# Kernel tuning notes

Measured on AMD Instinct MI355X. Metric: run time of the kernel, lower is better.

Reference implementation:

```python
import jax, jax.numpy as jnp
import numpy as np

EMBED = 1024
HEADS = 16
HEAD_DIM = EMBED // HEADS
N, L = 2, 2048


def setup_inputs() -> dict:
    key = jax.random.key(0)
    ks = jax.random.split(key, 9)
    s = 0.02
    return {
        "values": jax.random.normal(ks[0], (N, L, EMBED), jnp.float32),
        "key": jax.random.normal(ks[1], (N, L, EMBED), jnp.float32),
        "query": jax.random.normal(ks[2], (N, L, EMBED), jnp.float32),
        "mask": jnp.ones((N, 1, 1, L), jnp.int32),
        "Wv": jax.random.normal(ks[3], (HEAD_DIM, HEAD_DIM), jnp.float32) * s,
        "Wk": jax.random.normal(ks[4], (HEAD_DIM, HEAD_DIM), jnp.float32) * s,
        "Wq": jax.random.normal(ks[5], (HEAD_DIM, HEAD_DIM), jnp.float32) * s,
        "bq": jax.random.normal(ks[6], (HEAD_DIM,), jnp.float32) * s,
        "Wo": jax.random.normal(ks[7], (EMBED, EMBED), jnp.float32) * s,
        "bo": jax.random.normal(ks[8], (EMBED,), jnp.float32) * s,
    }


def reference(values, key, query, mask, Wv, Wk, Wq, bq, Wo, bo):
    n, q_len, E = query.shape
    D = Wv.shape[0]
    H = E // D
    # split heads: (N, len, H, D)
    v = values.reshape(n, -1, H, D)
    k = key.reshape(n, -1, H, D)
    q = query.reshape(n, q_len, H, D)
    # per-head linear projections (torch Linear: x @ W.T [+ b])
    v = jnp.einsum("nlhd,ed->nlhe", v, Wv)
    k = jnp.einsum("nlhd,ed->nlhe", k, Wk)
    q = jnp.einsum("nlhd,ed->nlhe", q, Wq) + bq
    # scores: (N, H, q_len, k_len)
    energy = jnp.einsum("nqhd,nkhd->nhqk", q, k)
    energy = jnp.where(mask == 0, jnp.float32(-1e20), energy)
    # NOTE: original scales by sqrt(embed_size), not sqrt(head_dim)
    attn = jax.nn.softmax(energy / jnp.sqrt(jnp.float32(E)), axis=-1)
    out = jnp.einsum("nhqk,nkhd->nqhd", attn, v).reshape(n, q_len, E)
    return out @ Wo.T + bo
```

## Files before the change

### kernel.cpp

```cpp
#include <hip/hip_runtime.h>
#include <hip/hip_bf16.h>
#include <string.h>

#define NB   2
#define SEQ  2048
#define EMB  1024
#define NH   16
#define HD   64
#define QSCALE 0.045084219f
#define MADD2  -4.5084219e18f

typedef __attribute__((ext_vector_type(8))) short short8;
typedef __attribute__((ext_vector_type(4))) float f32x4;

#define MFMA(a, b, c) __builtin_amdgcn_mfma_f32_16x16x32_bf16(a, b, c, 0, 0, 0)
#define EXP2(x) __builtin_amdgcn_exp2f(x)

__device__ __forceinline__ unsigned short f2bf(float x) {
    union { float f; unsigned u; } v; v.f = x;
    unsigned r = v.u + 0x7fffu + ((v.u >> 16) & 1u);
    return (unsigned short)(r >> 16);
}
__device__ __forceinline__ unsigned packbf2(float a, float b) {
    __hip_bfloat162 h = __float22bfloat162_rn(make_float2(a, b));
    unsigned u; memcpy(&u, &h, 4);
    return u;
}
__device__ __forceinline__ void gload16(const void* g, void* l) {
    __builtin_amdgcn_global_load_lds(
        (const __attribute__((address_space(1))) void*)g,
        (__attribute__((address_space(3))) void*)l, 16, 0, 0);
}

__global__ __launch_bounds__(256) void cvt_kernel(
    const float* __restrict__ Wo, const float* __restrict__ Wq,
    const float* __restrict__ Wk, const float* __restrict__ Wv,
    const int* __restrict__ mask,
    unsigned short* __restrict__ Wob, unsigned short* __restrict__ Wqb,
    unsigned short* __restrict__ Wkb, unsigned short* __restrict__ Wvb,
    float* __restrict__ maddG)
{
    const int b = blockIdx.x, tid = threadIdx.x;
    if (b < 1024) {
        int idx = b * 256 + tid;
        float4 w = ((const float4*)Wo)[idx];
        uint2 p; p.x = packbf2(w.x, w.y); p.y = packbf2(w.z, w.w);
        ((uint2*)Wob)[idx] = p;
    } else if (b < 1027) {
        const float* W = (b == 1024) ? Wq : (b == 1025) ? Wk : Wv;
        unsigned short* Wb = (b == 1024) ? Wqb : (b == 1025) ? Wkb : Wvb;
        #pragma unroll
        for (int i = 0; i < 4; ++i) {
            int idx = tid + i * 256;
            float4 w = ((const float4*)W)[idx];
            uint2 p; p.x = packbf2(w.x, w.y); p.y = packbf2(w.z, w.w);
            ((uint2*)Wb)[idx] = p;
        }
    } else {
        #pragma unroll
        for (int i = 0; i < 16; ++i) {
            int idx = tid + i * 256;
            maddG[idx] = mask[idx] ? 0.f : MADD2;
        }
    }
}

__global__ __launch_bounds__(256) void qkv_kernel(
    const float* __restrict__ Qin, const float* __restrict__ Kin,
    const float* __restrict__ Vin,
    const unsigned short* __restrict__ Wqb, const unsigned short* __restrict__ Wkb,
    const unsigned short* __restrict__ Wvb, const float* __restrict__ bq,
    unsigned short* __restrict__ Qp, unsigned short* __restrict__ Kp,
    unsigned short* __restrict__ Vtp)
{
    const int lt = blockIdx.x;
    const int h  = blockIdx.y;
    const int tz = blockIdx.z;
    const int t  = tz >> 1, n = tz & 1;

    const float* X; const unsigned short* Wb;
    if (t == 0)      { X = Qin; Wb = Wqb; }
    else if (t == 1) { X = Kin; Wb = Wkb; }
    else             { X = Vin; Wb = Wvb; }

    __shared__ __align__(16) unsigned short sX[128][70];
    __shared__ __align__(16) unsigned short sT[64][136];

    const int tid = threadIdx.x, wave = tid >> 6, lane = tid & 63;
    const int ln = lane & 15, quad = lane >> 4;

    #pragma unroll
    for (int i = 0; i < 8; ++i) {
        int flat = tid + i * 256;
        int r = flat >> 4, c4 = flat & 15;
        float4 xv = *(const float4*)(X + ((size_t)(n * SEQ + lt * 128 + r)) * EMB + h * HD + c4 * 4);
        uint2 xp; xp.x = packbf2(xv.x, xv.y); xp.y = packbf2(xv.z, xv.w);
        *(uint2*)&sX[r][c4 * 4] = xp;
    }
    short8 wf0[4], wf1[4];
    #pragma unroll
    for (int nt = 0; nt < 4; ++nt) {
        wf0[nt] = *(const short8*)(Wb + (nt * 16 + ln) * HD + quad * 8);
        wf1[nt] = *(const short8*)(Wb + (nt * 16 + ln) * HD + 32 + quad * 8);
    }
    __syncthreads();

    f32x4 acc[2][4];
    #pragma unroll
    for (int set = 0; set < 2; ++set) {
        short8 af0 = *(const short8*)&sX[wave * 32 + set * 16 + ln][quad * 8];
        short8 af1 = *(const short8*)&sX[wave * 32 + set * 16 + ln][32 + quad * 8];
        #pragma unroll
        for (int nt = 0; nt < 4; ++nt) {
            f32x4 a = {0.f, 0.f, 0.f, 0.f};
            a = MFMA(af0, wf0[nt], a);
            a = MFMA(af1, wf1[nt], a);
            acc[set][nt] = a;
        }
    }

    if (t == 0) {
        #pragma unroll
        for (int nt = 0; nt < 4; ++nt) {
            float bb = bq[nt * 16 + ln];
            #pragma unroll
            for (int set = 0; set < 2; ++set)
                #pragma unroll
                for (int a = 0; a < 4; ++a)
                    acc[set][nt][a] = (acc[set][nt][a] + bb) * QSCALE;
        }
    }

    if (t < 2) {
        unsigned short* Out = (t == 0) ? Qp : Kp;
        #pragma unroll
        for (int set = 0; set < 2; ++set)
            #pragma unroll
            for (int a = 0; a < 4; ++a) {
                size_t row = (size_t)((n * NH + h) * SEQ + lt * 128 + wave * 32 + set * 16 + quad * 4 + a);
                #pragma unroll
                for (int nt = 0; nt < 4; ++nt)
                    Out[row * HD + nt * 16 + ln] = f2bf(acc[set][nt][a]);
            }
    } else {
        #pragma unroll
        for (int set = 0; set < 2; ++set)
            #pragma unroll
            for (int nt = 0; nt < 4; ++nt)
                #pragma unroll
                for (int a = 0; a < 4; ++a)
                    sT[nt * 16 + ln][wave * 32 + set * 16 + quad * 4 + a] = f2bf(acc[set][nt][a]);
        __syncthreads();
        #pragma unroll
        for (int i = 0; i < 4; ++i) {
            int flat = tid + i * 256;
            int r = flat >> 4, c8 = flat & 15;
            *(float4*)(Vtp + ((size_t)((n * NH + h) * HD + r)) * SEQ + lt * 128 + c8 * 8) =
                *(const float4*)&sT[r][c8 * 8];
        }
    }
}

__global__ __launch_bounds__(256) void flash_kernel(
    const unsigned short* __restrict__ Qp, const unsigned short* __restrict__ Kp,
    const unsigned short* __restrict__ Vtp, const float* __restrict__ maddG,
    unsigned short* __restrict__ A )
{
    const int nh = blockIdx.x;
    const int qt = blockIdx.y;
    const int n  = nh >> 4, h = nh & 15;

    const int tid  = threadIdx.x;
    const int wave = tid >> 6, lane = tid & 63;
    const int ln   = lane & 15, quad = lane >> 4;
    const int ln7  = lane & 7;

    __shared__ __align__(16) unsigned short Kb[2][64 * 64];
    __shared__ __align__(16) unsigned short Vb[2][64 * 64];
    __shared__ __align__(16) unsigned short sP[4][32 * 64];
    unsigned short* sPw = sP[wave];

    const unsigned short* Qb = Qp + ((size_t)nh * SEQ + qt * 128 + wave * 32) * HD;
    short8 qf[2][2];
    #pragma unroll
    for (int set = 0; set < 2; ++set) {
        qf[set][0] = *(const short8*)(Qb + (set * 16 + ln) * HD + quad * 8);
        qf[set][1] = *(const short8*)(Qb + (set * 16 + ln) * HD + 32 + quad * 8);
    }

    const unsigned short* Kg = Kp  + (size_t)nh * SEQ * HD;
    const unsigned short* Vg = Vtp + (size_t)nh * HD * SEQ;
    const float* mb = maddG + n * SEQ;

    const int r8  = lane >> 3;
    const int swz = ((lane & 7) ^ r8) << 3;

    f32x4 o[2][4];
    #pragma unroll
    for (int s2 = 0; s2 < 2; ++s2)
        #pragma unroll
        for (int dt = 0; dt < 4; ++dt) o[s2][dt] = (f32x4){0.f, 0.f, 0.f, 0.f};
    float lsum[2] = {0.f, 0.f};

    #define STAGE(buf, kt_) do {                                                  \
        const unsigned short* kg_ = Kg + ((size_t)((kt_) * 64 + wave * 16 + r8)) * HD + swz; \
        const unsigned short* vg_ = Vg + ((size_t)(wave * 16 + r8)) * SEQ + (kt_) * 64 + swz; \
        unsigned short* kl_ = &Kb[buf][wave * 16 * 64];                           \
        unsigned short* vl_ = &Vb[buf][wave * 16 * 64];                           \
        gload16(kg_,            kl_);                                             \
        gload16(kg_ + 8 * HD,   kl_ + 8 * 64);                                    \
        gload16(vg_,            vl_);                                             \
        gload16(vg_ + 8 * SEQ,  vl_ + 8 * 64);                                    \
    } while (0)

    STAGE(0, 0);
    __syncthreads();
    int cur = 0;

    for (int kt = 0; kt < SEQ / 64; ++kt) {
        float4 md[4];
        #pragma unroll
        for (int nt = 0; nt < 4; ++nt)
            md[nt] = *(const float4*)(mb + kt * 64 + nt * 16 + quad * 4);

        if (kt + 1 < SEQ / 64) STAGE(cur ^ 1, kt + 1);

        const unsigned short* Kc = Kb[cur];
        #pragma unroll
        for (int nt = 0; nt < 4; ++nt) {
            short8 kf0 = *(const short8*)&Kc[(nt * 16 + ln) * 64 + (((quad)     ^ ln7) << 3)];
            short8 kf1 = *(const short8*)&Kc[(nt * 16 + ln) * 64 + (((quad + 4) ^ ln7) << 3)];
            #pragma unroll
            for (int set = 0; set < 2; ++set) {
                f32x4 z = {0.f, 0.f, 0.f, 0.f};
                z = MFMA(kf0, qf[set][0], z);
                z = MFMA(kf1, qf[set][1], z);
                float p0 = EXP2(fminf(z[0] + md[nt].x, 80.f));
                float p1 = EXP2(fminf(z[1] + md[nt].y, 80.f));
                float p2 = EXP2(fminf(z[2] + md[nt].z, 80.f));
                float p3 = EXP2(fminf(z[3] + md[nt].w, 80.f));
                lsum[set] += (p0 + p1) + (p2 + p3);
                uint2 w; w.x = packbf2(p0, p1); w.y = packbf2(p2, p3);
                int prow  = set * 16 + ln;
                int chunk = nt * 2 + (quad >> 1);
                *(uint2*)&sPw[prow * 64 + ((chunk ^ ln7) << 3) + (quad & 1) * 4] = w;
            }
        }
        asm volatile("s_waitcnt lgkmcnt(0)" ::: "memory");

        const unsigned short* Vc = Vb[cur];
        short8 pf[2][2];
        #pragma unroll
        for (int set = 0; set < 2; ++set) {
            pf[set][0] = *(const short8*)&sPw[(set * 16 + ln) * 64 + (((quad)     ^ ln7) << 3)];
            pf[set][1] = *(const short8*)&sPw[(set * 16 + ln) * 64 + (((quad + 4) ^ ln7) << 3)];
        }
        #pragma unroll
        for (int dt = 0; dt < 4; ++dt) {
            short8 vf0 = *(const short8*)&Vc[(dt * 16 + ln) * 64 + (((quad)     ^ ln7) << 3)];
            short8 vf1 = *(const short8*)&Vc[(dt * 16 + ln) * 64 + (((quad + 4) ^ ln7) << 3)];
            #pragma unroll
            for (int set = 0; set < 2; ++set) {
                o[set][dt] = MFMA(pf[set][0], vf0, o[set][dt]);
                o[set][dt] = MFMA(pf[set][1], vf1, o[set][dt]);
            }
        }

        __syncthreads();
        cur ^= 1;
    }
    #undef STAGE

    #pragma unroll
    for (int set = 0; set < 2; ++set) {
        float l = lsum[set];
        l += __shfl_xor(l, 16);
        l += __shfl_xor(l, 32);
        #pragma unroll
        for (int a = 0; a < 4; ++a) {
            float inv = 1.0f / __shfl(l, quad * 4 + a);
            size_t row = (size_t)(n * SEQ + qt * 128 + wave * 32 + set * 16 + quad * 4 + a);
            #pragma unroll
            for (int dt = 0; dt < 4; ++dt)
                A[row * EMB + h * HD + dt * 16 + ln] = f2bf(o[set][dt][a] * inv);
        }
    }
}

__global__ __launch_bounds__(256) void outproj_kernel(
    const unsigned short* __restrict__ A, const unsigned short* __restrict__ Wob,
    const float* __restrict__ bo, float* __restrict__ Out)
{
    const int ct = blockIdx.x;
    const int rt = blockIdx.y;

    const int tid  = threadIdx.x;
    const int wave = tid >> 6, lane = tid & 63;
    const int ln   = lane & 15, quad = lane >> 4;
    const int wm   = wave >> 1, wn = wave & 1;

    __shared__ __align__(16) unsigned short sA[128][72];
    __shared__ __align__(16) unsigned short sB[128][72];

    f32x4 acc[4][4];
    #pragma unroll
    for (int i = 0; i < 4; ++i)
        #pragma unroll
        for (int j = 0; j < 4; ++j) acc[i][j] = (f32x4){0.f, 0.f, 0.f, 0.f};

    for (int kc = 0; kc < EMB / 64; ++kc) {
        __syncthreads();
        #pragma unroll
        for (int i = 0; i < 4; ++i) {
            int flat = tid + i * 256;
            int r = flat >> 3, c8 = flat & 7;
            *(float4*)&sA[r][c8 * 8] =
                *(const float4*)(A + (size_t)(rt * 128 + r) * EMB + kc * 64 + c8 * 8);
            *(float4*)&sB[r][c8 * 8] =
                *(const float4*)(Wob + (size_t)(ct * 128 + r) * EMB + kc * 64 + c8 * 8);
        }
        __syncthreads();

        #pragma unroll
        for (int ks = 0; ks < 2; ++ks) {
            short8 af[4], bf[4];
            #pragma unroll
            for (int i = 0; i < 4; ++i)
                af[i] = *(const short8*)&sA[wm * 64 + i * 16 + ln][ks * 32 + quad * 8];
            #pragma unroll
            for (int j = 0; j < 4; ++j)
                bf[j] = *(const short8*)&sB[wn * 64 + j * 16 + ln][ks * 32 + quad * 8];
            #pragma unroll
            for (int i = 0; i < 4; ++i)
                #pragma unroll
                for (int j = 0; j < 4; ++j)
                    acc[i][j] = MFMA(af[i], bf[j], acc[i][j]);
        }
    }

    #pragma unroll
    for (int j = 0; j < 4; ++j) {
        int col = ct * 128 + wn * 64 + j * 16 + ln;
        float bb = bo[col];
        #pragma unroll
        for (int i = 0; i < 4; ++i)
            #pragma unroll
            for (int a = 0; a < 4; ++a) {
                size_t row = (size_t)(rt * 128 + wm * 64 + i * 16 + quad * 4 + a);
                Out[row * EMB + col] = acc[i][j][a] + bb;
            }
    }
}

extern "C" void kernel_launch(void* const* d_in, const int* in_sizes, int n_in,
                              void* d_out, int out_size, void* d_ws, size_t ws_size,
                              hipStream_t stream) {
    const float* values = (const float*)d_in[0];
    const float* key_   = (const float*)d_in[1];
    const float* query  = (const float*)d_in[2];
    const int*   mask   = (const int*)d_in[3];
    const float* Wv     = (const float*)d_in[4];
    const float* Wk     = (const float*)d_in[5];
    const float* Wq     = (const float*)d_in[6];
    const float* bq     = (const float*)d_in[7];
    const float* Wo     = (const float*)d_in[8];
    const float* bo     = (const float*)d_in[9];
    float* out = (float*)d_out;

    const size_t NHLD = (size_t)NB * NH * SEQ * HD;

    unsigned short* ws = (unsigned short*)d_ws;
    unsigned short* Qp    = ws;
    unsigned short* Kp    = ws + NHLD;
    unsigned short* Vtp   = ws + 2 * NHLD;
    unsigned short* Aattn = ws + 3 * NHLD;
    unsigned short* Wob   = ws + 4 * NHLD;
    unsigned short* Wqb   = Wob + (size_t)EMB * EMB;
    unsigned short* Wkb   = Wqb + HD * HD;
    unsigned short* Wvb   = Wkb + HD * HD;
    float* maddG = (float*)(Wvb + HD * HD);

    cvt_kernel<<<dim3(1028), 256, 0, stream>>>(
        Wo, Wq, Wk, Wv, mask, Wob, Wqb, Wkb, Wvb, maddG);
    qkv_kernel<<<dim3(SEQ / 128, NH, 3 * NB), 256, 0, stream>>>(
        query, key_, values, Wqb, Wkb, Wvb, bq, Qp, Kp, Vtp);
    flash_kernel<<<dim3(NB * NH, SEQ / 128), 256, 0, stream>>>(
        Qp, Kp, Vtp, maddG, Aattn);
    outproj_kernel<<<dim3(EMB / 128, NB * SEQ / 128), 256, 0, stream>>>(
        Aattn, Wob, bo, out);
}
```

Baseline: 205.1 us.

## Apply key mask by zeroing V rows and computing row sums with MFMA

Instead of adding a large negative bias before exp2 and clamping, the flash kernel now exponentiates raw scores. It applies the mask by zeroing masked rows of V in the projection kernel. It also computes the softmax denominator as P times a bf16 0/1 mask vector on the matrix cores. This removes the per-element add, min and scalar sum plus the final cross-lane shuffles from the inner loop, at the cost of extra MFMAs. Dropping the clamp risks overflow if scores are large, and the denominator is now summed from bf16-rounded probabilities.

```diff
diff --git a/kernel.cpp b/kernel.cpp
--- a/kernel.cpp
+++ b/kernel.cpp
@@ -8,7 +8,6 @@
 #define NH   16
 #define HD   64
 #define QSCALE 0.045084219f
-#define MADD2  -4.5084219e18f
 
 typedef __attribute__((ext_vector_type(8))) short short8;
 typedef __attribute__((ext_vector_type(4))) float f32x4;
@@ -38,7 +37,7 @@
     const int* __restrict__ mask,
     unsigned short* __restrict__ Wob, unsigned short* __restrict__ Wqb,
     unsigned short* __restrict__ Wkb, unsigned short* __restrict__ Wvb,
-    float* __restrict__ maddG)
+    unsigned short* __restrict__ Mb)
 {
     const int b = blockIdx.x, tid = threadIdx.x;
     if (b < 1024) {
@@ -60,7 +59,7 @@
         #pragma unroll
         for (int i = 0; i < 16; ++i) {
             int idx = tid + i * 256;
-            maddG[idx] = mask[idx] ? 0.f : MADD2;
+            Mb[idx] = mask[idx] ? (unsigned short)0x3F80 : (unsigned short)0;
         }
     }
 }
@@ -70,6 +69,7 @@
     const float* __restrict__ Vin,
     const unsigned short* __restrict__ Wqb, const unsigned short* __restrict__ Wkb,
     const unsigned short* __restrict__ Wvb, const float* __restrict__ bq,
+    const int* __restrict__ mask,
     unsigned short* __restrict__ Qp, unsigned short* __restrict__ Kp,
     unsigned short* __restrict__ Vtp)
 {
@@ -146,6 +146,16 @@
         #pragma unroll
         for (int set = 0; set < 2; ++set)
             #pragma unroll
+            for (int a = 0; a < 4; ++a) {
+                int l = lt * 128 + wave * 32 + set * 16 + quad * 4 + a;
+                if (mask[n * SEQ + l] == 0) {
+                    #pragma unroll
+                    for (int nt = 0; nt < 4; ++nt) acc[set][nt][a] = 0.f;
+                }
+            }
+        #pragma unroll
+        for (int set = 0; set < 2; ++set)
+            #pragma unroll
             for (int nt = 0; nt < 4; ++nt)
                 #pragma unroll
                 for (int a = 0; a < 4; ++a)
@@ -163,7 +173,7 @@
 
 __global__ __launch_bounds__(256) void flash_kernel(
     const unsigned short* __restrict__ Qp, const unsigned short* __restrict__ Kp,
-    const unsigned short* __restrict__ Vtp, const float* __restrict__ maddG,
+    const unsigned short* __restrict__ Vtp, const unsigned short* __restrict__ Mb,
     unsigned short* __restrict__ A )
 {
     const int nh = blockIdx.x;
@@ -190,7 +200,7 @@
 
     const unsigned short* Kg = Kp  + (size_t)nh * SEQ * HD;
     const unsigned short* Vg = Vtp + (size_t)nh * HD * SEQ;
-    const float* mb = maddG + n * SEQ;
+    const unsigned short* mk = Mb + n * SEQ;
 
     const int r8  = lane >> 3;
     const int swz = ((lane & 7) ^ r8) << 3;
@@ -200,7 +210,7 @@
     for (int s2 = 0; s2 < 2; ++s2)
         #pragma unroll
         for (int dt = 0; dt < 4; ++dt) o[s2][dt] = (f32x4){0.f, 0.f, 0.f, 0.f};
-    float lsum[2] = {0.f, 0.f};
+    f32x4 ol[2] = {(f32x4){0.f, 0.f, 0.f, 0.f}, (f32x4){0.f, 0.f, 0.f, 0.f}};
 
     #define STAGE(buf, kt_) do {                                                  \
         const unsigned short* kg_ = Kg + ((size_t)((kt_) * 64 + wave * 16 + r8)) * HD + swz; \
@@ -218,10 +228,8 @@
     int cur = 0;
 
     for (int kt = 0; kt < SEQ / 64; ++kt) {
-        float4 md[4];
-        #pragma unroll
-        for (int nt = 0; nt < 4; ++nt)
-            md[nt] = *(const float4*)(mb + kt * 64 + nt * 16 + quad * 4);
+        short8 mf0 = *(const short8*)(mk + kt * 64 + quad * 8);
+        short8 mf1 = *(const short8*)(mk + kt * 64 + 32 + quad * 8);
 
         if (kt + 1 < SEQ / 64) STAGE(cur ^ 1, kt + 1);
 
@@ -235,11 +243,10 @@
                 f32x4 z = {0.f, 0.f, 0.f, 0.f};
                 z = MFMA(kf0, qf[set][0], z);
                 z = MFMA(kf1, qf[set][1], z);
-                float p0 = EXP2(fminf(z[0] + md[nt].x, 80.f));
-                float p1 = EXP2(fminf(z[1] + md[nt].y, 80.f));
-                float p2 = EXP2(fminf(z[2] + md[nt].z, 80.f));
-                float p3 = EXP2(fminf(z[3] + md[nt].w, 80.f));
-                lsum[set] += (p0 + p1) + (p2 + p3);
+                float p0 = EXP2(z[0]);
+                float p1 = EXP2(z[1]);
+                float p2 = EXP2(z[2]);
+                float p3 = EXP2(z[3]);
                 uint2 w; w.x = packbf2(p0, p1); w.y = packbf2(p2, p3);
                 int prow  = set * 16 + ln;
                 int chunk = nt * 2 + (quad >> 1);
@@ -256,6 +263,11 @@
             pf[set][1] = *(const short8*)&sPw[(set * 16 + ln) * 64 + (((quad + 4) ^ ln7) << 3)];
         }
         #pragma unroll
+        for (int set = 0; set < 2; ++set) {
+            ol[set] = MFMA(pf[set][0], mf0, ol[set]);
+            ol[set] = MFMA(pf[set][1], mf1, ol[set]);
+        }
+        #pragma unroll
         for (int dt = 0; dt < 4; ++dt) {
             short8 vf0 = *(const short8*)&Vc[(dt * 16 + ln) * 64 + (((quad)     ^ ln7) << 3)];
             short8 vf1 = *(const short8*)&Vc[(dt * 16 + ln) * 64 + (((quad + 4) ^ ln7) << 3)];
@@ -272,19 +284,15 @@
     #undef STAGE
 
     #pragma unroll
-    for (int set = 0; set < 2; ++set) {
-        float l = lsum[set];
-        l += __shfl_xor(l, 16);
-        l += __shfl_xor(l, 32);
+    for (int set = 0; set < 2; ++set)
         #pragma unroll
         for (int a = 0; a < 4; ++a) {
-            float inv = 1.0f / __shfl(l, quad * 4 + a);
+            float inv = 1.0f / ol[set][a];
             size_t row = (size_t)(n * SEQ + qt * 128 + wave * 32 + set * 16 + quad * 4 + a);
             #pragma unroll
             for (int dt = 0; dt < 4; ++dt)
                 A[row * EMB + h * HD + dt * 16 + ln] = f2bf(o[set][dt][a] * inv);
         }
-    }
 }
 
 __global__ __launch_bounds__(256) void outproj_kernel(
@@ -378,14 +386,14 @@
     unsigned short* Wqb   = Wob + (size_t)EMB * EMB;
     unsigned short* Wkb   = Wqb + HD * HD;
     unsigned short* Wvb   = Wkb + HD * HD;
-    float* maddG = (float*)(Wvb + HD * HD);
+    unsigned short* Mb    = Wvb + HD * HD;
 
     cvt_kernel<<<dim3(1028), 256, 0, stream>>>(
-        Wo, Wq, Wk, Wv, mask, Wob, Wqb, Wkb, Wvb, maddG);
+        Wo, Wq, Wk, Wv, mask, Wob, Wqb, Wkb, Wvb, Mb);
     qkv_kernel<<<dim3(SEQ / 128, NH, 3 * NB), 256, 0, stream>>>(
-        query, key_, values, Wqb, Wkb, Wvb, bq, Qp, Kp, Vtp);
+        query, key_, values, Wqb, Wkb, Wvb, bq, mask, Qp, Kp, Vtp);
     flash_kernel<<<dim3(NB * NH, SEQ / 128), 256, 0, stream>>>(
-        Qp, Kp, Vtp, maddG, Aattn);
+        Qp, Kp, Vtp, Mb, Aattn);
     outproj_kernel<<<dim3(EMB / 128, NB * SEQ / 128), 256, 0, stream>>>(
         Aattn, Wob, bo, out);
 }
```

After: 192.9 us. -5.9%, faster.
